# Optimization experiments

Measured on AMD Instinct MI355X. Metric: run time of the kernel, lower is better.

## Reference

```python
import jax, jax.numpy as jnp
import numpy as np

B, C, H, W = 8, 256, 64, 64
CQK = C // 8


def setup_inputs() -> dict:
    key = jax.random.key(0)
    ks = jax.random.split(key, 9)
    s_in = 1.0 / np.sqrt(C)
    return {
        "feature1": jax.random.normal(ks[0], (B, C, H, W), jnp.float32),
        "feature2": jax.random.normal(ks[1], (B, C, H, W), jnp.float32),
        "feature3": jax.random.normal(ks[2], (B, C, H, W), jnp.float32),
        # 1x1 conv weights stored as [out_ch, in_ch]
        "wq": jax.random.uniform(ks[3], (CQK, C), jnp.float32, -s_in, s_in),
        "bq": jax.random.uniform(ks[4], (CQK,), jnp.float32, -s_in, s_in),
        "wk": jax.random.uniform(ks[5], (CQK, C), jnp.float32, -s_in, s_in),
        "bk": jax.random.uniform(ks[6], (CQK,), jnp.float32, -s_in, s_in),
        "wv": jax.random.uniform(ks[7], (C, C), jnp.float32, -s_in, s_in),
        "bv": jax.random.uniform(ks[8], (C,), jnp.float32, -s_in, s_in),
    }


def reference(feature1, feature2, feature3, wq, bq, wk, bk, wv, bv):
    b, c, h, w = feature1.shape
    hw = h * w
    # 1x1 convs == per-pixel channel GEMMs
    q = jnp.einsum('bchw,oc->bohw', feature1, wq) + bq[None, :, None, None]
    k = jnp.einsum('bchw,oc->bohw', feature2, wk) + bk[None, :, None, None]
    v = jnp.einsum('bchw,oc->bohw', feature3, wv) + bv[None, :, None, None]
    q = q.reshape(b, -1, hw).transpose(0, 2, 1)  # [b, hw, cqk]
    k = k.reshape(b, -1, hw)                      # [b, cqk, hw]
    v = v.reshape(b, -1, hw)                      # [b, c, hw]
    attn = jax.nn.softmax(jnp.einsum('bnc,bcm->bnm', q, k), axis=-1)  # [b, hw, hw]
    # fused = value @ attn^T  -> [b, c, hw]
    fused = jnp.einsum('bcm,bnm->bcn', v, attn)
    return fused.reshape(b, c, h, w)
```

## Files before the change

kernel.cpp:

```cpp
#include <hip/hip_runtime.h>
#include <math.h>

#define BATCH 8
#define CH    256
#define HWPIX 4096
#define CQK_  32

typedef __bf16 bf16x8 __attribute__((ext_vector_type(8)));
typedef __bf16 bf16x4 __attribute__((ext_vector_type(4)));
typedef __bf16 bf16x2 __attribute__((ext_vector_type(2)));
typedef float  f32x4  __attribute__((ext_vector_type(4)));

#define FS_STR 68

static __device__ inline bf16x8 ld_frag(const __bf16* p) {
  bf16x4 lo = *(const bf16x4*)p;
  bf16x4 hi = *(const bf16x4*)(p + 4);
  return __builtin_shufflevector(lo, hi, 0, 1, 2, 3, 4, 5, 6, 7);
}

static __device__ inline bf16x8 w_frag(const float* p) {
  const float4 a = *(const float4*)p;
  const float4 b = *(const float4*)(p + 4);
  bf16x8 r;
  r[0] = (__bf16)a.x; r[1] = (__bf16)a.y; r[2] = (__bf16)a.z; r[3] = (__bf16)a.w;
  r[4] = (__bf16)b.x; r[5] = (__bf16)b.y; r[6] = (__bf16)b.z; r[7] = (__bf16)b.w;
  return r;
}

__global__ __launch_bounds__(512, 4) void proj_all(
    const float* __restrict__ f1, const float* __restrict__ f2,
    const float* __restrict__ f3,
    const float* __restrict__ wq, const float* __restrict__ bq,
    const float* __restrict__ wk, const float* __restrict__ bk,
    const float* __restrict__ wv, const float* __restrict__ bv,
    __bf16* __restrict__ qT, __bf16* __restrict__ kT, __bf16* __restrict__ vv)
{
  __shared__ __align__(16) __bf16 f_s[2][128 * FS_STR];
  const int t    = threadIdx.x;
  const int w    = __builtin_amdgcn_readfirstlane(t >> 6);
  const int lane = t & 63;
  const int q16  = lane & 15;
  const int quad = lane >> 4;
  const int b    = blockIdx.z;
  const int n0   = blockIdx.x * 128;
  const int mode = blockIdx.y;

  if (mode == 0) {
    const int half = t >> 8;
    const int th   = t & 255;
    const int px   = (th & 31) * 4;
    const int g2   = (th >> 5) * 2;
    const int isK  = w >> 2;
    const int qr   = w & 3;

    const float* fsrc = (half ? f2 : f1) + (size_t)b * CH * HWPIX + n0;
    __bf16* fdst = f_s[half];
    const float* wmat = isK ? wk : wq;

    f32x4 acc[2][2];
#pragma unroll
    for (int i = 0; i < 2; ++i)
#pragma unroll
      for (int j = 0; j < 2; ++j) acc[i][j] = (f32x4){0.f, 0.f, 0.f, 0.f};

    float4 rg_[8];
#define PLOAD(c0)                                                               \
    _Pragma("unroll") for (int cc = 0; cc < 4; ++cc) {                          \
      const int c = (c0) + 16 * cc + g2;                                        \
      rg_[2 * cc]     = *(const float4*)&fsrc[(size_t)c * HWPIX + px];          \
      rg_[2 * cc + 1] = *(const float4*)&fsrc[(size_t)(c + 1) * HWPIX + px];    \
    }
    PLOAD(0);
    for (int c0 = 0; c0 < CH; c0 += 64) {
      __syncthreads();
#pragma unroll
      for (int cc = 0; cc < 4; ++cc) {
        const int c = 16 * cc + g2;
#pragma unroll
        for (int i = 0; i < 4; ++i) {
          bf16x2 pk;
          pk[0] = (__bf16)((const float*)&rg_[2 * cc])[i];
          pk[1] = (__bf16)((const float*)&rg_[2 * cc + 1])[i];
          *(bf16x2*)&fdst[(px + i) * FS_STR + c] = pk;
        }
      }
      __syncthreads();
      if (c0 < CH - 64) PLOAD(c0 + 64);
      bf16x8 af[2][2];
#pragma unroll
      for (int rg = 0; rg < 2; ++rg)
#pragma unroll
        for (int kh = 0; kh < 2; ++kh)
          af[rg][kh] = ld_frag(&f_s[isK][(32 * qr + 16 * rg + q16) * FS_STR
                                         + 32 * kh + quad * 8]);
#pragma unroll
      for (int ot = 0; ot < 2; ++ot)
#pragma unroll
        for (int kh = 0; kh < 2; ++kh) {
          const bf16x8 wf =
              w_frag(wmat + (size_t)(16 * ot + q16) * CH + c0 + 32 * kh + quad * 8);
#pragma unroll
          for (int rg = 0; rg < 2; ++rg)
            acc[ot][rg] = __builtin_amdgcn_mfma_f32_16x16x32_bf16(
                af[rg][kh], wf, acc[ot][rg], 0, 0, 0);
        }
    }
    const float* bias = isK ? bk : bq;
    __bf16* outT = isK ? kT : qT;
    const float b0 = bias[q16], b1 = bias[16 + q16];
#pragma unroll
    for (int rg = 0; rg < 2; ++rg)
#pragma unroll
      for (int r = 0; r < 4; ++r) {
        const size_t row = (size_t)b * HWPIX + n0 + 32 * qr + 16 * rg + quad * 4 + r;
        outT[row * CQK_ + q16]      = (__bf16)(acc[0][rg][r] + b0);
        outT[row * CQK_ + 16 + q16] = (__bf16)(acc[1][rg][r] + b1);
      }
#undef PLOAD
  } else {
    const int px = (t & 31) * 4;
    const int g2 = (t >> 5) * 2;
    const float* f3b = f3 + (size_t)b * CH * HWPIX + n0;

    f32x4 acc[2][8];
#pragma unroll
    for (int ct = 0; ct < 2; ++ct)
#pragma unroll
      for (int nt = 0; nt < 8; ++nt) acc[ct][nt] = (f32x4){0.f, 0.f, 0.f, 0.f};

    float4 r_[4];
#define VLOAD(c0)                                                               \
    _Pragma("unroll") for (int cc = 0; cc < 2; ++cc) {                          \
      const int c = (c0) + 32 * cc + g2;                                        \
      r_[2 * cc]     = *(const float4*)&f3b[(size_t)c * HWPIX + px];            \
      r_[2 * cc + 1] = *(const float4*)&f3b[(size_t)(c + 1) * HWPIX + px];      \
    }
    VLOAD(0);
    for (int c0 = 0; c0 < CH; c0 += 64) {
      __syncthreads();
#pragma unroll
      for (int cc = 0; cc < 2; ++cc) {
        const int c = 32 * cc + g2;
#pragma unroll
        for (int i = 0; i < 4; ++i) {
          bf16x2 pk;
          pk[0] = (__bf16)((const float*)&r_[2 * cc])[i];
          pk[1] = (__bf16)((const float*)&r_[2 * cc + 1])[i];
          *(bf16x2*)&f_s[0][(px + i) * FS_STR + c] = pk;
        }
      }
      __syncthreads();
      if (c0 < CH - 64) VLOAD(c0 + 64);
      bf16x8 af[2][2];
#pragma unroll
      for (int ct = 0; ct < 2; ++ct)
#pragma unroll
        for (int kh = 0; kh < 2; ++kh)
          af[ct][kh] = w_frag(wv + (size_t)(32 * w + 16 * ct + q16) * CH
                              + c0 + 32 * kh + quad * 8);
#pragma unroll
      for (int nt = 0; nt < 8; ++nt) {
#pragma unroll
        for (int kh = 0; kh < 2; ++kh) {
          const bf16x8 bfr =
              ld_frag(&f_s[0][(16 * nt + q16) * FS_STR + 32 * kh + quad * 8]);
#pragma unroll
          for (int ct = 0; ct < 2; ++ct)
            acc[ct][nt] = __builtin_amdgcn_mfma_f32_16x16x32_bf16(
                af[ct][kh], bfr, acc[ct][nt], 0, 0, 0);
        }
      }
    }
#pragma unroll
    for (int ct = 0; ct < 2; ++ct) {
      const float4 bi = *(const float4*)&bv[32 * w + 16 * ct + quad * 4];
#pragma unroll
      for (int nt = 0; nt < 8; ++nt) {
#pragma unroll
        for (int r = 0; r < 4; ++r) {
          const int c = 32 * w + 16 * ct + quad * 4 + r;
          vv[((size_t)b * CH + c) * HWPIX + n0 + 16 * nt + q16] =
              (__bf16)(acc[ct][nt][r] + ((const float*)&bi)[r]);
        }
      }
    }
#undef VLOAD
  }
}

__global__ __launch_bounds__(512, 4) void attn_kernel(
    const __bf16* __restrict__ qT, const __bf16* __restrict__ kT,
    const __bf16* __restrict__ vv, float* __restrict__ out)
{
  __shared__ __align__(16) __bf16 p_s[2][64 * 128];
  __shared__ float L_s[2][64];

  const int t    = threadIdx.x;
  const int w    = __builtin_amdgcn_readfirstlane(t >> 6);
  const int lane = t & 63;
  const int q16  = lane & 15;
  const int quad = lane >> 4;
  const int qb   = w & 3;
  const int hb   = w >> 2;
  const int swz  = (q16 & 7) << 4;

  const int b  = blockIdx.x & 7;
  const int q0 = (blockIdx.x >> 3) * 64;

  const __bf16* kTb = kT + (size_t)b * HWPIX * CQK_;
  const size_t koff = (size_t)(32 * hb + q16) * CQK_ + quad * 8;

  const __bf16* vp[2];
#pragma unroll
  for (int ct = 0; ct < 2; ++ct)
    vp[ct] = vv + ((size_t)b * CH + 32 * w + 16 * ct + q16) * HWPIX + quad * 8;

  const bf16x8 qfrag =
      *(const bf16x8*)(qT + ((size_t)b * HWPIX + q0 + 16 * qb + q16) * CQK_ + quad * 8);

  f32x4 oacc[2][4];
#pragma unroll
  for (int i = 0; i < 2; ++i)
#pragma unroll
    for (int j = 0; j < 4; ++j)
      oacc[i][j] = (f32x4){0.f, 0.f, 0.f, 0.f};
  float Lp = 0.f;

  bf16x8 kf[4];
#pragma unroll
  for (int tm = 0; tm < 4; ++tm)
    kf[tm] = *(const bf16x8*)(kTb + (size_t)(tm >> 1) * 2048 + (tm & 1) * 512 + koff);
  {
    f32x4 Sv[4];
#pragma unroll
    for (int tm = 0; tm < 4; ++tm)
      Sv[tm] = __builtin_amdgcn_mfma_f32_16x16x32_bf16(
          kf[tm], qfrag, (f32x4){0.f, 0.f, 0.f, 0.f}, 0, 0, 0);
    const __bf16* kb1 = kTb + 4096;
#pragma unroll
    for (int tm = 0; tm < 4; ++tm)
      kf[tm] = *(const bf16x8*)(kb1 + (size_t)(tm >> 1) * 2048 + (tm & 1) * 512 + koff);
    char* pw = (char*)p_s[0] + (16 * qb + q16) * 256;
#pragma unroll
    for (int tm = 0; tm < 4; ++tm) {
      bf16x4 pk;
#pragma unroll
      for (int r = 0; r < 4; ++r) {
        const float e = __expf(Sv[tm][r]);
        Lp += e;
        pk[r] = (__bf16)e;
      }
      *(bf16x4*)(pw + ((128 * (tm >> 1) + 64 * hb + 32 * (tm & 1) + 8 * quad) ^ swz)) = pk;
    }
  }
  __syncthreads();

  for (int i = 0; i < 32; ++i) {
    bf16x8 vf[2][4];
#pragma unroll
    for (int ct = 0; ct < 2; ++ct)
#pragma unroll
      for (int mh = 0; mh < 4; ++mh)
        vf[ct][mh] = *(const bf16x8*)(vp[ct] + mh * 32);

    const char* pb = (const char*)p_s[i & 1];

    if (i < 31) {
      f32x4 Sv[4];
#pragma unroll
      for (int tm = 0; tm < 4; ++tm)
        Sv[tm] = __builtin_amdgcn_mfma_f32_16x16x32_bf16(
            kf[tm], qfrag, (f32x4){0.f, 0.f, 0.f, 0.f}, 0, 0, 0);
      const __bf16* kb2 = kTb + (size_t)((i + 2) & 31) * 4096;
#pragma unroll
      for (int tm = 0; tm < 4; ++tm)
        kf[tm] = *(const bf16x8*)(kb2 + (size_t)(tm >> 1) * 2048 + (tm & 1) * 512 + koff);
      char* pw = (char*)p_s[(i + 1) & 1] + (16 * qb + q16) * 256;
#pragma unroll
      for (int tm = 0; tm < 4; ++tm) {
        bf16x4 pk;
#pragma unroll
        for (int r = 0; r < 4; ++r) {
          const float e = __expf(Sv[tm][r]);
          Lp += e;
          pk[r] = (__bf16)e;
        }
        *(bf16x4*)(pw + ((128 * (tm >> 1) + 64 * hb + 32 * (tm & 1) + 8 * quad) ^ swz)) = pk;
      }
    }

#pragma unroll
    for (int mh = 0; mh < 4; ++mh) {
      bf16x8 pf[4];
#pragma unroll
      for (int nt = 0; nt < 4; ++nt)
        pf[nt] = *(const bf16x8*)(pb + (16 * nt + q16) * 256
                                  + ((64 * mh + 16 * quad) ^ swz));
#pragma unroll
      for (int ct = 0; ct < 2; ++ct)
#pragma unroll
        for (int nt = 0; nt < 4; ++nt)
          oacc[ct][nt] = __builtin_amdgcn_mfma_f32_16x16x32_bf16(
              vf[ct][mh], pf[nt], oacc[ct][nt], 0, 0, 0);
    }

#pragma unroll
    for (int ct = 0; ct < 2; ++ct) vp[ct] += 128;
    __syncthreads();
  }

  Lp += __shfl_xor(Lp, 16);
  Lp += __shfl_xor(Lp, 32);
  if (quad == 0) L_s[hb][16 * qb + q16] = Lp;
  __syncthreads();

  float rinv[4];
#pragma unroll
  for (int nt = 0; nt < 4; ++nt)
    rinv[nt] = 1.0f / (L_s[0][16 * nt + q16] + L_s[1][16 * nt + q16]);

  float* ob = out + ((size_t)b * CH + 32 * w) * HWPIX + q0;
#pragma unroll
  for (int ct = 0; ct < 2; ++ct)
#pragma unroll
    for (int r = 0; r < 4; ++r)
#pragma unroll
      for (int nt = 0; nt < 4; ++nt)
        ob[(size_t)(16 * ct + quad * 4 + r) * HWPIX + 16 * nt + q16] =
            oacc[ct][nt][r] * rinv[nt];
}

extern "C" void kernel_launch(void* const* d_in, const int* in_sizes, int n_in,
                              void* d_out, int out_size, void* d_ws, size_t ws_size,
                              hipStream_t stream)
{
  const float* f1 = (const float*)d_in[0];
  const float* f2 = (const float*)d_in[1];
  const float* f3 = (const float*)d_in[2];
  const float* wq = (const float*)d_in[3];
  const float* bq = (const float*)d_in[4];
  const float* wk = (const float*)d_in[5];
  const float* bk = (const float*)d_in[6];
  const float* wv = (const float*)d_in[7];
  const float* bv = (const float*)d_in[8];
  float* outp = (float*)d_out;

  __bf16* qTw = (__bf16*)d_ws;
  __bf16* kTw = qTw + (size_t)BATCH * HWPIX * CQK_;
  __bf16* vw  = kTw + (size_t)BATCH * HWPIX * CQK_;

  proj_all<<<dim3(32, 2, 8), 512, 0, stream>>>(f1, f2, f3, wq, bq, wk, bk, wv, bv,
                                               qTw, kTw, vw);
  attn_kernel<<<dim3(512), 512, 0, stream>>>(qTw, kTw, vw, outp);
}
```

Before: 295.6 us.

## Halve key tile to 64 and stagger key-tile start per query block

Shrinks the key tile per iteration from 128 to 64 pixels, which halves the shared-memory P buffer and doubles the loop count to 64 iterations. Each query block starts its key/value sweep at a different offset (qt & 63), so blocks running concurrently read different parts of K and V and contend less on the same memory channels. The P fragments are now loaded before the score computation so the LDS reads can overlap it. The cost is twice as many barriers per block and less work between them.

Result: no change. 293.8 us (-0.6%).

```diff
diff --git a/kernel.cpp b/kernel.cpp
--- a/kernel.cpp
+++ b/kernel.cpp
@@ -193,7 +193,7 @@
     const __bf16* __restrict__ qT, const __bf16* __restrict__ kT,
     const __bf16* __restrict__ vv, float* __restrict__ out)
 {
-  __shared__ __align__(16) __bf16 p_s[2][64 * 128];
+  __shared__ __align__(16) __bf16 p_s[2][64 * 64];
   __shared__ float L_s[2][64];
 
   const int t    = threadIdx.x;
@@ -205,16 +205,18 @@
   const int hb   = w >> 2;
   const int swz  = (q16 & 7) << 4;
 
-  const int b  = blockIdx.x & 7;
-  const int q0 = (blockIdx.x >> 3) * 64;
+  const int b    = blockIdx.x & 7;
+  const int qt   = blockIdx.x >> 3;
+  const int q0   = qt * 64;
+  const int ioff = qt & 63;
 
   const __bf16* kTb = kT + (size_t)b * HWPIX * CQK_;
   const size_t koff = (size_t)(32 * hb + q16) * CQK_ + quad * 8;
 
-  const __bf16* vp[2];
+  const __bf16* vb[2];
 #pragma unroll
   for (int ct = 0; ct < 2; ++ct)
-    vp[ct] = vv + ((size_t)b * CH + 32 * w + 16 * ct + q16) * HWPIX + quad * 8;
+    vb[ct] = vv + ((size_t)b * CH + 32 * w + 16 * ct + q16) * HWPIX + quad * 8;
 
   const bf16x8 qfrag =
       *(const bf16x8*)(qT + ((size_t)b * HWPIX + q0 + 16 * qb + q16) * CQK_ + quad * 8);
@@ -227,86 +229,87 @@
       oacc[i][j] = (f32x4){0.f, 0.f, 0.f, 0.f};
   float Lp = 0.f;
 
-  bf16x8 kf[4];
-#pragma unroll
-  for (int tm = 0; tm < 4; ++tm)
-    kf[tm] = *(const bf16x8*)(kTb + (size_t)(tm >> 1) * 2048 + (tm & 1) * 512 + koff);
+  bf16x8 kf[2];
+#pragma unroll
+  for (int mt = 0; mt < 2; ++mt)
+    kf[mt] = *(const bf16x8*)(kTb + (size_t)ioff * (64 * CQK_) + koff + mt * 512);
   {
-    f32x4 Sv[4];
-#pragma unroll
-    for (int tm = 0; tm < 4; ++tm)
-      Sv[tm] = __builtin_amdgcn_mfma_f32_16x16x32_bf16(
-          kf[tm], qfrag, (f32x4){0.f, 0.f, 0.f, 0.f}, 0, 0, 0);
-    const __bf16* kb1 = kTb + 4096;
-#pragma unroll
-    for (int tm = 0; tm < 4; ++tm)
-      kf[tm] = *(const bf16x8*)(kb1 + (size_t)(tm >> 1) * 2048 + (tm & 1) * 512 + koff);
-    char* pw = (char*)p_s[0] + (16 * qb + q16) * 256;
-#pragma unroll
-    for (int tm = 0; tm < 4; ++tm) {
+    f32x4 Sv[2];
+#pragma unroll
+    for (int mt = 0; mt < 2; ++mt)
+      Sv[mt] = __builtin_amdgcn_mfma_f32_16x16x32_bf16(
+          kf[mt], qfrag, (f32x4){0.f, 0.f, 0.f, 0.f}, 0, 0, 0);
+    const __bf16* kb1 = kTb + (size_t)((ioff + 1) & 63) * (64 * CQK_);
+#pragma unroll
+    for (int mt = 0; mt < 2; ++mt)
+      kf[mt] = *(const bf16x8*)(kb1 + koff + mt * 512);
+    char* pw = (char*)p_s[0] + (16 * qb + q16) * 128;
+#pragma unroll
+    for (int mt = 0; mt < 2; ++mt) {
       bf16x4 pk;
 #pragma unroll
       for (int r = 0; r < 4; ++r) {
-        const float e = __expf(Sv[tm][r]);
+        const float e = __expf(Sv[mt][r]);
         Lp += e;
         pk[r] = (__bf16)e;
       }
-      *(bf16x4*)(pw + ((128 * (tm >> 1) + 64 * hb + 32 * (tm & 1) + 8 * quad) ^ swz)) = pk;
+      *(bf16x4*)(pw + ((64 * hb + 32 * mt + 8 * quad) ^ swz)) = pk;
     }
   }
   __syncthreads();
 
-  for (int i = 0; i < 32; ++i) {
-    bf16x8 vf[2][4];
+  for (int i = 0; i < 64; ++i) {
+    const int jj = (i + ioff) & 63;
+
+    bf16x8 vf[2][2];
 #pragma unroll
     for (int ct = 0; ct < 2; ++ct)
 #pragma unroll
-      for (int mh = 0; mh < 4; ++mh)
-        vf[ct][mh] = *(const bf16x8*)(vp[ct] + mh * 32);
+      for (int mh = 0; mh < 2; ++mh)
+        vf[ct][mh] = *(const bf16x8*)(vb[ct] + jj * 64 + mh * 32);
 
     const char* pb = (const char*)p_s[i & 1];
-
-    if (i < 31) {
-      f32x4 Sv[4];
-#pragma unroll
-      for (int tm = 0; tm < 4; ++tm)
-        Sv[tm] = __builtin_amdgcn_mfma_f32_16x16x32_bf16(
-            kf[tm], qfrag, (f32x4){0.f, 0.f, 0.f, 0.f}, 0, 0, 0);
-      const __bf16* kb2 = kTb + (size_t)((i + 2) & 31) * 4096;
-#pragma unroll
-      for (int tm = 0; tm < 4; ++tm)
-        kf[tm] = *(const bf16x8*)(kb2 + (size_t)(tm >> 1) * 2048 + (tm & 1) * 512 + koff);
-      char* pw = (char*)p_s[(i + 1) & 1] + (16 * qb + q16) * 256;
-#pragma unroll
-      for (int tm = 0; tm < 4; ++tm) {
+    bf16x8 pf[4][2];
+#pragma unroll
+    for (int nt = 0; nt < 4; ++nt)
+#pragma unroll
+      for (int mh = 0; mh < 2; ++mh)
+        pf[nt][mh] = *(const bf16x8*)(pb + (16 * nt + q16) * 128
+                                      + ((64 * mh + 16 * quad) ^ swz));
+
+    if (i < 63) {
+      f32x4 Sv[2];
+#pragma unroll
+      for (int mt = 0; mt < 2; ++mt)
+        Sv[mt] = __builtin_amdgcn_mfma_f32_16x16x32_bf16(
+            kf[mt], qfrag, (f32x4){0.f, 0.f, 0.f, 0.f}, 0, 0, 0);
+      const __bf16* kb2 = kTb + (size_t)((i + 2 + ioff) & 63) * (64 * CQK_);
+#pragma unroll
+      for (int mt = 0; mt < 2; ++mt)
+        kf[mt] = *(const bf16x8*)(kb2 + koff + mt * 512);
+      char* pw = (char*)p_s[(i + 1) & 1] + (16 * qb + q16) * 128;
+#pragma unroll
+      for (int mt = 0; mt < 2; ++mt) {
         bf16x4 pk;
 #pragma unroll
         for (int r = 0; r < 4; ++r) {
-          const float e = __expf(Sv[tm][r]);
+          const float e = __expf(Sv[mt][r]);
           Lp += e;
           pk[r] = (__bf16)e;
         }
-        *(bf16x4*)(pw + ((128 * (tm >> 1) + 64 * hb + 32 * (tm & 1) + 8 * quad) ^ swz)) = pk;
-      }
-    }
-
-#pragma unroll
-    for (int mh = 0; mh < 4; ++mh) {
-      bf16x8 pf[4];
+        *(bf16x4*)(pw + ((64 * hb + 32 * mt + 8 * quad) ^ swz)) = pk;
+      }
+    }
+
+#pragma unroll
+    for (int ct = 0; ct < 2; ++ct)
 #pragma unroll
       for (int nt = 0; nt < 4; ++nt)
-        pf[nt] = *(const bf16x8*)(pb + (16 * nt + q16) * 256
-                                  + ((64 * mh + 16 * quad) ^ swz));
-#pragma unroll
-      for (int ct = 0; ct < 2; ++ct)
-#pragma unroll
-        for (int nt = 0; nt < 4; ++nt)
+#pragma unroll
+        for (int mh = 0; mh < 2; ++mh)
           oacc[ct][nt] = __builtin_amdgcn_mfma_f32_16x16x32_bf16(
-              vf[ct][mh], pf[nt], oacc[ct][nt], 0, 0, 0);
-    }
-
-#pragma unroll
-    for (int ct = 0; ct < 2; ++ct) vp[ct] += 128;
+              vf[ct][mh], pf[nt][mh], oacc[ct][nt], 0, 0, 0);
+
     __syncthreads();
   }
 
```
